# Kernel tuning notes

Measured on AMD Instinct MI355X. Metric: run time of the kernel, lower is better.

The kernel has to match this reference:

```python
import jax, jax.numpy as jnp
import numpy as np

B, L, W, C = 16, 200, 64, 128
H_INTRA = 64   # intra_hidden // 2 per direction
H_INTER = 128
EPS = 1e-8


def layer_norm(x, gamma, beta):
    mu = jnp.mean(x, axis=-1, keepdims=True)
    var = jnp.mean(jnp.square(x - mu), axis=-1, keepdims=True)
    return (x - mu) * jax.lax.rsqrt(var + EPS) * gamma + beta


def gru_seq(x, Wk, Uk, b, H):
    """Keras GRU, reset_after=False, recurrent_activation=sigmoid. x: [N,T,D] -> [N,T,H]."""
    xw = jnp.einsum('ntd,dk->ntk', x, Wk) + b  # precompute input projections [N,T,3H]
    def step(h, xw_t):
        z = jax.nn.sigmoid(xw_t[:, :H] + h @ Uk[:, :H])
        r = jax.nn.sigmoid(xw_t[:, H:2 * H] + h @ Uk[:, H:2 * H])
        hh = jnp.tanh(xw_t[:, 2 * H:] + (r * h) @ Uk[:, 2 * H:])
        h = z * h + (1.0 - z) * hh
        return h, h
    h0 = jnp.zeros((x.shape[0], H), x.dtype)
    _, ys = jax.lax.scan(step, h0, jnp.swapaxes(xw, 0, 1))  # [T,N,H]
    return jnp.swapaxes(ys, 0, 1)


def skip_gru_seq(x, Wk, Uk, b, Wp, bp, H):
    """Skip-RNN GRU (Campos et al.): binary update gate u_t conditionally updates state.
    Returns (outputs [N,T,H], gates [N,T,1])."""
    xw = jnp.einsum('ntd,dk->ntk', x, Wk) + b
    def step(carry, xw_t):
        h, ut = carry
        # straight-through binarization of cumulative update prob
        u = ut + jax.lax.stop_gradient(jnp.round(ut) - ut)  # [N,1]
        z = jax.nn.sigmoid(xw_t[:, :H] + h @ Uk[:, :H])
        r = jax.nn.sigmoid(xw_t[:, H:2 * H] + h @ Uk[:, H:2 * H])
        hh = jnp.tanh(xw_t[:, 2 * H:] + (r * h) @ Uk[:, 2 * H:])
        h_new = z * h + (1.0 - z) * hh
        h = u * h_new + (1.0 - u) * h  # skip: copy state when u == 0
        delta = jax.nn.sigmoid(h @ Wp + bp)  # [N,1]
        ut_next = u * delta + (1.0 - u) * (ut + jnp.minimum(delta, 1.0 - ut))
        return (h, ut_next), (h, u)
    N = x.shape[0]
    h0 = jnp.zeros((N, H), x.dtype)
    ut0 = jnp.ones((N, 1), x.dtype)
    _, (ys, us) = jax.lax.scan(step, (h0, ut0), jnp.swapaxes(xw, 0, 1))
    return jnp.swapaxes(ys, 0, 1), jnp.swapaxes(us, 0, 1)


def setup_inputs():
    key = jax.random.key(0)
    ks = jax.random.split(key, 16)
    rn = lambda k, s: jax.random.normal(k, s, dtype=jnp.float32) * 0.05
    z = lambda s: jnp.zeros(s, jnp.float32)
    o = lambda s: jnp.ones(s, jnp.float32)
    return {
        'x': jax.random.normal(ks[0], (B, L, W, C), dtype=jnp.float32),
        'scale': jax.random.uniform(ks[1], (B, L, W, 1), dtype=jnp.float32),
        'Wf': rn(ks[2], (C, 3 * H_INTRA)), 'Uf': rn(ks[3], (H_INTRA, 3 * H_INTRA)), 'bf': z((3 * H_INTRA,)),
        'Wb': rn(ks[4], (C, 3 * H_INTRA)), 'Ub': rn(ks[5], (H_INTRA, 3 * H_INTRA)), 'bb': z((3 * H_INTRA,)),
        'W_intra_fc': rn(ks[6], (2 * H_INTRA, C)), 'b_intra_fc': z((C,)),
        'g_intra': o((C,)), 'beta_intra': z((C,)),
        'Wi': rn(ks[7], (C + 1, 3 * H_INTER)), 'Ui': rn(ks[8], (H_INTER, 3 * H_INTER)), 'bi': z((3 * H_INTER,)),
        'Wp': rn(ks[9], (H_INTER, 1)), 'bp': z((1,)),
        'W_inter_fc': rn(ks[10], (H_INTER, C)), 'b_inter_fc': z((C,)),
        'g_inter': o((C,)), 'beta_inter': z((C,)),
    }


def reference(x, scale, Wf, Uf, bf, Wb, Ub, bb, W_intra_fc, b_intra_fc, g_intra, beta_intra,
              Wi, Ui, bi, Wp, bp, W_inter_fc, b_inter_fc, g_inter, beta_inter):
    # ----- intra path: bidirectional GRU over the width axis -----
    intra_in = x.reshape(B * L, W, C)
    out_f = gru_seq(intra_in, Wf, Uf, bf, H_INTRA)
    out_b = gru_seq(intra_in[:, ::-1, :], Wb, Ub, bb, H_INTRA)[:, ::-1, :]
    intra_rnn_out = jnp.concatenate([out_f, out_b], axis=-1)  # [B*L, W, 2H]
    update_gate_intra = jnp.ones((64, L), jnp.float32)  # skip=0 branch: constant ones
    intra_dense = intra_rnn_out @ W_intra_fc + b_intra_fc  # [B*L, W, C]
    intra_out = x + layer_norm(intra_dense.reshape(B, L, W, C), g_intra, beta_intra)
    # ----- inter path: skip-GRU over the L (time) axis -----
    inter_in = jnp.transpose(intra_out, (0, 2, 1, 3)).reshape(B * W, L, C)
    scale2 = jnp.transpose(scale, (0, 2, 1, 3)).reshape(B * W, L, 1)
    inter_in = jnp.concatenate([inter_in, scale2], axis=-1)  # [B*W, L, C+1]
    inter_rnn_out, gates = skip_gru_seq(inter_in, Wi, Ui, bi, Wp, bp, H_INTER)
    update_gate_inter = gates[:, :, 0]  # [B*W, L]
    inter_dense = (inter_rnn_out @ W_inter_fc + b_inter_fc).reshape(B, W, L, C)
    inter_ln_in = jnp.transpose(inter_dense, (0, 2, 1, 3))  # [B, L, W, C]
    inter_out = intra_out + layer_norm(inter_ln_in, g_inter, beta_inter)
    return inter_out, update_gate_intra, update_gate_inter
```

## Files before the change

### kernel.cpp

```cpp
#include <hip/hip_runtime.h>
#include <cmath>


__device__ __forceinline__ float sigf(float x) { return 1.0f / (1.0f + expf(-x)); }

__global__ __launch_bounds__(256) void k_fill_ones(float* __restrict__ p, int n) {
  int i = blockIdx.x * 256 + threadIdx.x;
  if (i < n) p[i] = 1.0f;
}

enum { MA_X_FWD = 0, MA_X_BWD = 1, MA_INTER = 2 };

template <int MODE>
__global__ __launch_bounds__(256) void k_gemm_xw(
    const float* __restrict__ A0, const float* __restrict__ A1,
    const float* __restrict__ Bm, const float* __restrict__ bias,
    float* __restrict__ Cm, long M0, int N, int K, int KT)
{
  __shared__ float As[16][68];
  __shared__ float Bs[16][68];
  const int tid = threadIdx.x;
  const int tx = tid & 15, ty = tid >> 4;
  const long row0g = M0 + (long)blockIdx.x * 64;
  const int col0 = blockIdx.y * 64;
  const int lr = tid >> 2;
  const int lk4 = (tid & 3) * 4;
  const int bk = tid >> 4;
  const int bc4 = (tid & 15) * 4;
  float acc[4][4];
#pragma unroll
  for (int i = 0; i < 4; ++i)
#pragma unroll
    for (int j = 0; j < 4; ++j) acc[i][j] = 0.f;

  for (int kt = 0; kt < KT; ++kt) {
    const int k0 = kt * 16;
    {
      const long rg = row0g + lr;
      float v0, v1, v2, v3;
      if (MODE == MA_X_FWD) {
        const float4 a4 = *reinterpret_cast<const float4*>(&A0[rg * 128 + k0 + lk4]);
        v0 = a4.x; v1 = a4.y; v2 = a4.z; v3 = a4.w;
      } else if (MODE == MA_X_BWD) {
        const long s = rg >> 6; const int t = (int)(rg & 63);
        const float4 a4 =
            *reinterpret_cast<const float4*>(&A0[(s * 64 + (63 - t)) * 128 + k0 + lk4]);
        v0 = a4.x; v1 = a4.y; v2 = a4.z; v3 = a4.w;
      } else {
        const int n = (int)(rg & 1023);
        const int l = (int)(rg >> 10);
        const long rowc = ((long)(n >> 6) * 200 + l) * 64 + (n & 63);
        const long base = rowc * 128;
        float vv[4];
#pragma unroll
        for (int i = 0; i < 4; ++i) {
          const int k = k0 + lk4 + i;
          vv[i] = (k < 128) ? A0[base + k] : ((k == 128) ? A1[rowc] : 0.f);
        }
        v0 = vv[0]; v1 = vv[1]; v2 = vv[2]; v3 = vv[3];
      }
      As[lk4 + 0][lr] = v0;
      As[lk4 + 1][lr] = v1;
      As[lk4 + 2][lr] = v2;
      As[lk4 + 3][lr] = v3;
    }
    {
      const int k = k0 + bk;
      float4 b4 = make_float4(0.f, 0.f, 0.f, 0.f);
      if (k < K) b4 = *reinterpret_cast<const float4*>(&Bm[(long)k * N + col0 + bc4]);
      *reinterpret_cast<float4*>(&Bs[bk][bc4]) = b4;
    }
    __syncthreads();
#pragma unroll
    for (int kk = 0; kk < 16; ++kk) {
      const float4 a4 = *reinterpret_cast<const float4*>(&As[kk][ty * 4]);
      const float4 b4 = *reinterpret_cast<const float4*>(&Bs[kk][tx * 4]);
      const float av[4] = {a4.x, a4.y, a4.z, a4.w};
      const float bv[4] = {b4.x, b4.y, b4.z, b4.w};
#pragma unroll
      for (int i = 0; i < 4; ++i)
#pragma unroll
        for (int j = 0; j < 4; ++j) acc[i][j] = fmaf(av[i], bv[j], acc[i][j]);
    }
    __syncthreads();
  }
  const float4 bi4 = *reinterpret_cast<const float4*>(&bias[col0 + tx * 4]);
  const float bv[4] = {bi4.x, bi4.y, bi4.z, bi4.w};
#pragma unroll
  for (int i = 0; i < 4; ++i) {
    const long rl = (long)blockIdx.x * 64 + ty * 4 + i;
    float4 o;
    o.x = acc[i][0] + bv[0];
    o.y = acc[i][1] + bv[1];
    o.z = acc[i][2] + bv[2];
    o.w = acc[i][3] + bv[3];
    *reinterpret_cast<float4*>(&Cm[rl * (long)N + col0 + tx * 4]) = o;
  }
}

__global__ __launch_bounds__(256, 2) void k_gru_intra(
    const float* __restrict__ xwf, const float* __restrict__ xwb,
    const float* __restrict__ Uf, const float* __restrict__ Ub,
    float* __restrict__ rnn, int nseq)
{
  const int dir = blockIdx.y;
  const float* __restrict__ xw = dir ? xwb : xwf;
  const float* __restrict__ U = dir ? Ub : Uf;
  __shared__ float Us[64 * 192];
  __shared__ float hs[8][64];
  __shared__ float zs[8][64];
  __shared__ float rhs[8][64];
  const int tid = threadIdx.x;
#pragma unroll
  for (int i = 0; i < 12; ++i) {
    *reinterpret_cast<float4*>(&Us[(tid + i * 256) * 4]) =
        *reinterpret_cast<const float4*>(&U[(tid + i * 256) * 4]);
  }
  reinterpret_cast<float*>(hs)[tid] = 0.f;
  reinterpret_cast<float*>(hs)[tid + 256] = 0.f;
  __syncthreads();
  const int sA = tid >> 5;
  const int cA = tid & 31;
  const long s0 = (long)blockIdx.x * 8;
  const long xbase = (s0 + sA) * 64;
  float4 xzr = *reinterpret_cast<const float4*>(&xw[(xbase + 0) * 192 + 4 * cA]);
  float2 xh = *reinterpret_cast<const float2*>(&xw[(xbase + 0) * 192 + 128 + 2 * cA]);
  for (int t = 0; t < 64; ++t) {
    float4 xzr_n = make_float4(0.f, 0.f, 0.f, 0.f);
    float2 xh_n = make_float2(0.f, 0.f);
    if (t < 63) {
      xzr_n = *reinterpret_cast<const float4*>(&xw[(xbase + t + 1) * 192 + 4 * cA]);
      xh_n = *reinterpret_cast<const float2*>(&xw[(xbase + t + 1) * 192 + 128 + 2 * cA]);
    }
    float a0 = 0.f, a1 = 0.f, a2 = 0.f, a3 = 0.f;
#pragma unroll
    for (int k4 = 0; k4 < 16; ++k4) {
      const float4 h4 = *reinterpret_cast<const float4*>(&hs[sA][4 * k4]);
      const float hv[4] = {h4.x, h4.y, h4.z, h4.w};
#pragma unroll
      for (int i = 0; i < 4; ++i) {
        const float4 u4 =
            *reinterpret_cast<const float4*>(&Us[(4 * k4 + i) * 192 + 4 * cA]);
        a0 = fmaf(hv[i], u4.x, a0);
        a1 = fmaf(hv[i], u4.y, a1);
        a2 = fmaf(hv[i], u4.z, a2);
        a3 = fmaf(hv[i], u4.w, a3);
      }
    }
    if (cA < 16) {
      float4 zq;
      zq.x = sigf(xzr.x + a0);
      zq.y = sigf(xzr.y + a1);
      zq.z = sigf(xzr.z + a2);
      zq.w = sigf(xzr.w + a3);
      *reinterpret_cast<float4*>(&zs[sA][4 * cA]) = zq;
    } else {
      const int j0 = 4 * cA - 64;
      const float4 h4 = *reinterpret_cast<const float4*>(&hs[sA][j0]);
      float4 rq;
      rq.x = sigf(xzr.x + a0) * h4.x;
      rq.y = sigf(xzr.y + a1) * h4.y;
      rq.z = sigf(xzr.z + a2) * h4.z;
      rq.w = sigf(xzr.w + a3) * h4.w;
      *reinterpret_cast<float4*>(&rhs[sA][j0]) = rq;
    }
    __syncthreads();
    float b0 = 0.f, b1 = 0.f;
#pragma unroll
    for (int k4 = 0; k4 < 16; ++k4) {
      const float4 r4 = *reinterpret_cast<const float4*>(&rhs[sA][4 * k4]);
      const float rv[4] = {r4.x, r4.y, r4.z, r4.w};
#pragma unroll
      for (int i = 0; i < 4; ++i) {
        const float2 u2 =
            *reinterpret_cast<const float2*>(&Us[(4 * k4 + i) * 192 + 128 + 2 * cA]);
        b0 = fmaf(rv[i], u2.x, b0);
        b1 = fmaf(rv[i], u2.y, b1);
      }
    }
    {
      const int j0 = 2 * cA;
      const float hh0 = tanhf(xh.x + b0);
      const float hh1 = tanhf(xh.y + b1);
      const float z0 = zs[sA][j0], z1 = zs[sA][j0 + 1];
      const float ho0 = hs[sA][j0], ho1 = hs[sA][j0 + 1];
      const float hn0 = z0 * ho0 + (1.f - z0) * hh0;
      const float hn1 = z1 * ho1 + (1.f - z1) * hh1;
      hs[sA][j0] = hn0;
      hs[sA][j0 + 1] = hn1;
      const int tt = dir ? (63 - t) : t;
      float2 st; st.x = hn0; st.y = hn1;
      *reinterpret_cast<float2*>(
          &rnn[((s0 + sA) * 64 + tt) * 128 + dir * 64 + j0]) = st;
    }
    __syncthreads();
    xzr = xzr_n; xh = xh_n;
  }
}

__global__ __launch_bounds__(512, 4) void k_gru_inter2(
    const float* __restrict__ xw, const float* __restrict__ Ui,
    const float* __restrict__ Wp, const float* __restrict__ bp,
    float* __restrict__ rnn, float* __restrict__ gates,
    float* __restrict__ hstate, float* __restrict__ ustate,
    int t0, int nt)
{
  __shared__ float Uh[128 * 128];
  __shared__ float h_s[2][128];
  __shared__ float z_s[2][128];
  __shared__ float rh_s[2][128];
  __shared__ float wp_s[128];
  __shared__ float pred[2][4];
  __shared__ float ut_s[2];
  __shared__ float u_s[2];
  const int tid = threadIdx.x;
  const int w = tid >> 6, lane = tid & 63, half = lane >> 5, lcol = lane & 31;
  const int n0 = blockIdx.x * 2;
  const int colA = w * 32 + lcol;
  const int ksA = half;
  const int seqB = w >> 2;
  const int colB = (w & 3) * 32 + lcol;
  const int ksB = half;

  float uzr[64];
#pragma unroll
  for (int k = 0; k < 64; ++k) uzr[k] = Ui[(long)(ksA * 64 + k) * 384 + colA];

  for (int idx = tid; idx < 16384; idx += 512) {
    const int k = idx >> 7, c = idx & 127;
    const float v = Ui[(long)k * 384 + 256 + c];
    Uh[c * 128 + (((k >> 2) ^ (c & 31)) << 2) + (k & 3)] = v;
  }
  if (tid < 256) {
    const int s = tid >> 7, c = tid & 127;
    h_s[s][c] = (t0 == 0) ? 0.f : hstate[(long)(n0 + s) * 128 + c];
  }
  if (tid < 128) wp_s[tid] = Wp[tid];
  if (tid < 2) {
    ut_s[tid] = (t0 == 0) ? 1.0f : ustate[n0 + tid];
    u_s[tid] = (t0 == 0) ? 1.0f : ustate[1024 + n0 + tid];
  }
  const float bp0 = bp[0];
  __syncthreads();

  float xa0 = 0.f, xa1 = 0.f, xb0 = 0.f;
  if (lane < 32) {
    xa0 = xw[(long)n0 * 384 + colA];
    xa1 = xw[(long)(n0 + 1) * 384 + colA];
    xb0 = xw[(long)(n0 + seqB) * 384 + 256 + colB];
  }

  for (int dl = 0; dl < nt; ++dl) {
    const int dn = (dl + 1 < nt) ? dl + 1 : dl;
    float xa0n = 0.f, xa1n = 0.f, xbn = 0.f;
    if (lane < 32) {
      xa0n = xw[((long)dn * 1024 + n0) * 384 + colA];
      xa1n = xw[((long)dn * 1024 + n0 + 1) * 384 + colA];
      xbn = xw[((long)dn * 1024 + n0 + seqB) * 384 + 256 + colB];
    }
    float a0 = 0.f, a1 = 0.f;
    const int hb = ksA * 64;
#pragma unroll
    for (int k4 = 0; k4 < 16; ++k4) {
      const float4 h0 = *reinterpret_cast<const float4*>(&h_s[0][hb + 4 * k4]);
      const float4 h1 = *reinterpret_cast<const float4*>(&h_s[1][hb + 4 * k4]);
      a0 = fmaf(h0.x, uzr[4 * k4 + 0], a0);
      a0 = fmaf(h0.y, uzr[4 * k4 + 1], a0);
      a0 = fmaf(h0.z, uzr[4 * k4 + 2], a0);
      a0 = fmaf(h0.w, uzr[4 * k4 + 3], a0);
      a1 = fmaf(h1.x, uzr[4 * k4 + 0], a1);
      a1 = fmaf(h1.y, uzr[4 * k4 + 1], a1);
      a1 = fmaf(h1.z, uzr[4 * k4 + 2], a1);
      a1 = fmaf(h1.w, uzr[4 * k4 + 3], a1);
    }
    a0 += __shfl_xor(a0, 32);
    a1 += __shfl_xor(a1, 32);
    if (lane < 32) {
      const float p0 = xa0 + a0;
      const float p1 = xa1 + a1;
      if (colA < 128) {
        z_s[0][colA] = sigf(p0);
        z_s[1][colA] = sigf(p1);
      } else {
        const int c = colA - 128;
        rh_s[0][c] = sigf(p0) * h_s[0][c];
        rh_s[1][c] = sigf(p1) * h_s[1][c];
      }
    }
    __syncthreads();
    float b = 0.f;
    const int rb = ksB * 64;
#pragma unroll
    for (int k4 = 0; k4 < 16; ++k4) {
      const float4 r4 = *reinterpret_cast<const float4*>(&rh_s[seqB][rb + 4 * k4]);
      const int chunk = ((ksB << 4) + k4) ^ (colB & 31);
      const float4 u4 = *reinterpret_cast<const float4*>(&Uh[colB * 128 + (chunk << 2)]);
      b = fmaf(r4.x, u4.x, b);
      b = fmaf(r4.y, u4.y, b);
      b = fmaf(r4.z, u4.z, b);
      b = fmaf(r4.w, u4.w, b);
    }
    b += __shfl_xor(b, 32);
    if (lane < 32) {
      const float pre = xb0 + b;
      const float hh = tanhf(pre);
      const float z = z_s[seqB][colB];
      const float ho = h_s[seqB][colB];
      const float hn = z * ho + (1.f - z) * hh;
      const float u = u_s[seqB];
      const float hq = u * hn + (1.f - u) * ho;
      rnn[((long)dl * 1024 + n0 + seqB) * 128 + colB] = hq;
      h_s[seqB][colB] = hq;
      float p = hq * wp_s[colB];
      p += __shfl_xor(p, 16);
      p += __shfl_xor(p, 8);
      p += __shfl_xor(p, 4);
      p += __shfl_xor(p, 2);
      p += __shfl_xor(p, 1);
      if (lcol == 0) pred[seqB][w & 3] = p;
    }
    __syncthreads();
    if (tid < 2) {
      const float pp = pred[tid][0] + pred[tid][1] + pred[tid][2] + pred[tid][3];
      const float delta = sigf(pp + bp0);
      const float u = u_s[tid], ut = ut_s[tid];
      gates[(long)(n0 + tid) * 200 + t0 + dl] = u;
      const float utn = u * delta + (1.f - u) * (ut + fminf(delta, 1.f - ut));
      ut_s[tid] = utn;
      u_s[tid] = rintf(utn);
    }
    xa0 = xa0n; xa1 = xa1n; xb0 = xbn;
  }
  if (tid < 256) {
    const int s = tid >> 7, c = tid & 127;
    hstate[(long)(n0 + s) * 128 + c] = h_s[s][c];
  }
  if (tid < 2) {
    ustate[n0 + tid] = ut_s[tid];
    ustate[1024 + n0 + tid] = u_s[tid];
  }
}

template <int OM>
__global__ __launch_bounds__(256) void k_fcln(
    const float* __restrict__ A, const float* __restrict__ Wt,
    const float* __restrict__ bias, const float* __restrict__ gamma,
    const float* __restrict__ beta, const float* __restrict__ resid,
    float* __restrict__ dst, long M0)
{
  __shared__ float As[16][36];
  __shared__ float Bs[16][132];
  __shared__ float red0[32][33];
  __shared__ float red1[32][33];
  __shared__ float mu_s[32];
  __shared__ float rs_s[32];
  const int tid = threadIdx.x;
  const int tx = tid & 31, ty = tid >> 5;
  const long r0l = (long)blockIdx.x * 32;
  const int lr = tid >> 3;
  const int lk2 = (tid & 7) * 2;
  const int bkk = tid >> 4;
  const int bc8 = (tid & 15) * 8;
  float acc[4][4];
#pragma unroll
  for (int i = 0; i < 4; ++i)
#pragma unroll
    for (int j = 0; j < 4; ++j) acc[i][j] = 0.f;

  for (int kt = 0; kt < 8; ++kt) {
    const int k0 = kt * 16;
    const float2 a2 = *reinterpret_cast<const float2*>(&A[(r0l + lr) * 128 + k0 + lk2]);
    As[lk2][lr] = a2.x;
    As[lk2 + 1][lr] = a2.y;
    const float4 w0 = *reinterpret_cast<const float4*>(&Wt[(long)(k0 + bkk) * 128 + bc8]);
    const float4 w1 = *reinterpret_cast<const float4*>(&Wt[(long)(k0 + bkk) * 128 + bc8 + 4]);
    *reinterpret_cast<float4*>(&Bs[bkk][bc8]) = w0;
    *reinterpret_cast<float4*>(&Bs[bkk][bc8 + 4]) = w1;
    __syncthreads();
#pragma unroll
    for (int kk = 0; kk < 16; ++kk) {
      const float4 a4 = *reinterpret_cast<const float4*>(&As[kk][ty * 4]);
      const float4 b4 = *reinterpret_cast<const float4*>(&Bs[kk][tx * 4]);
      const float av[4] = {a4.x, a4.y, a4.z, a4.w};
      const float bv[4] = {b4.x, b4.y, b4.z, b4.w};
#pragma unroll
      for (int i = 0; i < 4; ++i)
#pragma unroll
        for (int j = 0; j < 4; ++j) acc[i][j] = fmaf(av[i], bv[j], acc[i][j]);
    }
    __syncthreads();
  }
  {
    const float4 bb4 = *reinterpret_cast<const float4*>(&bias[tx * 4]);
    const float bv[4] = {bb4.x, bb4.y, bb4.z, bb4.w};
#pragma unroll
    for (int i = 0; i < 4; ++i)
#pragma unroll
      for (int j = 0; j < 4; ++j) acc[i][j] += bv[j];
  }
#pragma unroll
  for (int i = 0; i < 4; ++i) {
    const float s = acc[i][0] + acc[i][1] + acc[i][2] + acc[i][3];
    const float q = acc[i][0] * acc[i][0] + acc[i][1] * acc[i][1] +
                    acc[i][2] * acc[i][2] + acc[i][3] * acc[i][3];
    red0[ty * 4 + i][tx] = s;
    red1[ty * 4 + i][tx] = q;
  }
  __syncthreads();
  if (tid < 32) {
    float s = 0.f, q = 0.f;
#pragma unroll
    for (int j = 0; j < 32; ++j) { s += red0[tid][j]; q += red1[tid][j]; }
    const float mu = s * (1.0f / 128.0f);
    const float var = q * (1.0f / 128.0f) - mu * mu;
    mu_s[tid] = mu;
    rs_s[tid] = 1.0f / sqrtf(var + 1e-8f);
  }
  __syncthreads();
  const float4 g4 = *reinterpret_cast<const float4*>(&gamma[tx * 4]);
  const float4 be4 = *reinterpret_cast<const float4*>(&beta[tx * 4]);
#pragma unroll
  for (int i = 0; i < 4; ++i) {
    const int rloc = ty * 4 + i;
    const long rg = M0 + r0l + rloc;
    long off;
    if (OM == 0) {
      off = rg * 128 + tx * 4;
    } else {
      const int n = (int)(rg & 1023);
      const int l = (int)(rg >> 10);
      off = (((long)(n >> 6) * 200 + l) * 64 + (n & 63)) * 128 + tx * 4;
    }
    const float4 r4 = *reinterpret_cast<const float4*>(&resid[off]);
    const float mu = mu_s[rloc], rs = rs_s[rloc];
    float4 o;
    o.x = (acc[i][0] - mu) * rs * g4.x + be4.x + r4.x;
    o.y = (acc[i][1] - mu) * rs * g4.y + be4.y + r4.y;
    o.z = (acc[i][2] - mu) * rs * g4.z + be4.z + r4.z;
    o.w = (acc[i][3] - mu) * rs * g4.w + be4.w + r4.w;
    *reinterpret_cast<float4*>(&dst[off]) = o;
  }
}

extern "C" void kernel_launch(void* const* d_in, const int* in_sizes, int n_in,
                              void* d_out, int out_size, void* d_ws, size_t ws_size,
                              hipStream_t stream)
{
  (void)in_sizes; (void)n_in; (void)out_size;
  const float* x    = (const float*)d_in[0];
  const float* scl  = (const float*)d_in[1];
  const float* Wf   = (const float*)d_in[2];
  const float* Uf   = (const float*)d_in[3];
  const float* bf   = (const float*)d_in[4];
  const float* Wb   = (const float*)d_in[5];
  const float* Ub   = (const float*)d_in[6];
  const float* bb   = (const float*)d_in[7];
  const float* Wfc1 = (const float*)d_in[8];
  const float* bfc1 = (const float*)d_in[9];
  const float* gam1 = (const float*)d_in[10];
  const float* bet1 = (const float*)d_in[11];
  const float* Wi   = (const float*)d_in[12];
  const float* Ui   = (const float*)d_in[13];
  const float* bi   = (const float*)d_in[14];
  const float* Wp   = (const float*)d_in[15];
  const float* bp   = (const float*)d_in[16];
  const float* Wfc2 = (const float*)d_in[17];
  const float* bfc2 = (const float*)d_in[18];
  const float* gam2 = (const float*)d_in[19];
  const float* bet2 = (const float*)d_in[20];

  float* outp  = (float*)d_out;
  float* io    = outp;
  float* onesp = outp + 26214400L;
  float* gates = outp + 26214400L + 12800L;
  float* ws    = (float*)d_ws;
  const long wsf = (long)(ws_size / sizeof(float));

  k_fill_ones<<<50, 256, 0, stream>>>(onesp, 12800);

  long cnI = (wsf / 32768L) & ~7L;
  if (cnI > 3200) cnI = 3200;
  if (cnI < 8) cnI = 8;
  for (long s0 = 0; s0 < 3200; s0 += cnI) {
    const long cn = (3200 - s0 < cnI) ? (3200 - s0) : cnI;
    float* xwf = ws;
    float* xwb = ws + cn * 12288L;
    float* rnn = ws + cn * 24576L;
    const long M = cn * 64;
    dim3 gg((unsigned)(M / 64), 3);
    k_gemm_xw<MA_X_FWD><<<gg, 256, 0, stream>>>(x, nullptr, Wf, bf, xwf, s0 * 64, 192, 128, 8);
    k_gemm_xw<MA_X_BWD><<<gg, 256, 0, stream>>>(x, nullptr, Wb, bb, xwb, s0 * 64, 192, 128, 8);
    dim3 gr((unsigned)(cn / 8), 2);
    k_gru_intra<<<gr, 256, 0, stream>>>(xwf, xwb, Uf, Ub, rnn, (int)cn);
    k_fcln<0><<<(unsigned)(M / 32), 256, 0, stream>>>(rnn, Wfc1, bfc1, gam1, bet1, x, io, s0 * 64);
  }

  const long per_t = 1024L * 384 + 1024L * 128;
  const long state_f = 1024L * 128 + 2048L;
  long nt_alloc = (wsf - state_f) / per_t;
  if (nt_alloc > 200) nt_alloc = 200;
  if (nt_alloc < 1) nt_alloc = 1;
  float* xwi    = ws;
  float* rnnI   = ws + nt_alloc * 1024L * 384;
  float* hstate = rnnI + nt_alloc * 1024L * 128;
  float* ustate = hstate + 1024L * 128;

  for (long t0 = 0; t0 < 200; t0 += nt_alloc) {
    const int nt = (int)((200 - t0 < nt_alloc) ? (200 - t0) : nt_alloc);
    dim3 gg((unsigned)(16 * nt), 6);
    k_gemm_xw<MA_INTER><<<gg, 256, 0, stream>>>(io, scl, Wi, bi, xwi, t0 * 1024, 384, 129, 9);
    k_gru_inter2<<<512, 512, 0, stream>>>(xwi, Ui, Wp, bp, rnnI, gates, hstate, ustate,
                                          (int)t0, nt);
    k_fcln<1><<<(unsigned)(32 * nt), 256, 0, stream>>>(rnnI, Wfc2, bfc2, gam2, bet2, io, outp,
                                                       t0 * 1024);
  }
}
```

Baseline: 2.112 ms.

## Rewrite GRU recurrences with register-resident weights and readlane broadcast of state

Both recurrent kernels now keep the recurrent weight slices in per-wave registers and broadcast hidden-state elements across lanes with readlane, instead of streaming the weights from shared memory. K is split across waves and the partial sums are reduced through shared memory. The intra kernel handles 4 sequences per block. The inter kernel handles 4 sequences per block with 1024 threads and skips the matmuls for sequences whose binary update gate is zero. The inter input GEMM also replaces per-element guarded loads with vector loads, and the state workspace size is adjusted. In exchange there are more barriers per step and heavy register pressure (64 weight floats per thread), which may limit occupancy.

```diff
diff --git a/kernel.cpp b/kernel.cpp
--- a/kernel.cpp
+++ b/kernel.cpp
@@ -3,6 +3,9 @@
 
 
 __device__ __forceinline__ float sigf(float x) { return 1.0f / (1.0f + expf(-x)); }
+__device__ __forceinline__ float rlanef(float v, int l) {
+  return __uint_as_float(__builtin_amdgcn_readlane(__float_as_uint(v), (unsigned)l));
+}
 
 __global__ __launch_bounds__(256) void k_fill_ones(float* __restrict__ p, int n) {
   int i = blockIdx.x * 256 + threadIdx.x;
@@ -51,13 +54,13 @@
         const int l = (int)(rg >> 10);
         const long rowc = ((long)(n >> 6) * 200 + l) * 64 + (n & 63);
         const long base = rowc * 128;
-        float vv[4];
-#pragma unroll
-        for (int i = 0; i < 4; ++i) {
-          const int k = k0 + lk4 + i;
-          vv[i] = (k < 128) ? A0[base + k] : ((k == 128) ? A1[rowc] : 0.f);
-        }
-        v0 = vv[0]; v1 = vv[1]; v2 = vv[2]; v3 = vv[3];
+        if (kt < 8) {
+          const float4 a4 = *reinterpret_cast<const float4*>(&A0[base + k0 + lk4]);
+          v0 = a4.x; v1 = a4.y; v2 = a4.z; v3 = a4.w;
+        } else {
+          v0 = (lk4 == 0) ? A1[rowc] : 0.f;
+          v1 = 0.f; v2 = 0.f; v3 = 0.f;
+        }
       }
       As[lk4 + 0][lr] = v0;
       As[lk4 + 1][lr] = v1;
@@ -98,246 +101,284 @@
   }
 }
 
-__global__ __launch_bounds__(256, 2) void k_gru_intra(
+__global__ __launch_bounds__(256, 4) void k_gru_intra2(
     const float* __restrict__ xwf, const float* __restrict__ xwb,
     const float* __restrict__ Uf, const float* __restrict__ Ub,
-    float* __restrict__ rnn, int nseq)
+    float* __restrict__ rnn)
 {
   const int dir = blockIdx.y;
   const float* __restrict__ xw = dir ? xwb : xwf;
-  const float* __restrict__ U = dir ? Ub : Uf;
-  __shared__ float Us[64 * 192];
-  __shared__ float hs[8][64];
-  __shared__ float zs[8][64];
-  __shared__ float rhs[8][64];
+  const float* __restrict__ U  = dir ? Ub : Uf;
+  __shared__ float h8[4][64], z8[4][64], rh8[4][64];
+  __shared__ float pA[4][2][128];
+  __shared__ float pB[4][2][64];
   const int tid = threadIdx.x;
-#pragma unroll
-  for (int i = 0; i < 12; ++i) {
-    *reinterpret_cast<float4*>(&Us[(tid + i * 256) * 4]) =
-        *reinterpret_cast<const float4*>(&U[(tid + i * 256) * 4]);
-  }
-  reinterpret_cast<float*>(hs)[tid] = 0.f;
-  reinterpret_cast<float*>(hs)[tid + 256] = 0.f;
+  const int w = tid >> 6, lane = tid & 63;
+  const long s0 = (long)blockIdx.x * 4;
+  const bool isZR = (w < 2);
+  const int ksZ = w;
+  const int ksH = w - 2;
+
+  float ua[32], ub[32];
+  if (isZR) {
+#pragma unroll
+    for (int k = 0; k < 32; ++k) {
+      ua[k] = U[(ksZ * 32 + k) * 192 + lane];
+      ub[k] = U[(ksZ * 32 + k) * 192 + 64 + lane];
+    }
+  } else {
+#pragma unroll
+    for (int k = 0; k < 32; ++k)
+      ua[k] = U[(ksH * 32 + k) * 192 + 128 + lane];
+  }
+  h8[w][lane] = 0.f;
   __syncthreads();
-  const int sA = tid >> 5;
-  const int cA = tid & 31;
-  const long s0 = (long)blockIdx.x * 8;
-  const long xbase = (s0 + sA) * 64;
-  float4 xzr = *reinterpret_cast<const float4*>(&xw[(xbase + 0) * 192 + 4 * cA]);
-  float2 xh = *reinterpret_cast<const float2*>(&xw[(xbase + 0) * 192 + 128 + 2 * cA]);
+
+  const long xrow0 = (s0 + w) * 64;
+  float xa1 = xw[xrow0 * 192 + lane];
+  float xa2 = xw[xrow0 * 192 + 64 + lane];
+  float xb  = xw[xrow0 * 192 + 128 + lane];
+
   for (int t = 0; t < 64; ++t) {
-    float4 xzr_n = make_float4(0.f, 0.f, 0.f, 0.f);
-    float2 xh_n = make_float2(0.f, 0.f);
-    if (t < 63) {
-      xzr_n = *reinterpret_cast<const float4*>(&xw[(xbase + t + 1) * 192 + 4 * cA]);
-      xh_n = *reinterpret_cast<const float2*>(&xw[(xbase + t + 1) * 192 + 128 + 2 * cA]);
-    }
-    float a0 = 0.f, a1 = 0.f, a2 = 0.f, a3 = 0.f;
-#pragma unroll
-    for (int k4 = 0; k4 < 16; ++k4) {
-      const float4 h4 = *reinterpret_cast<const float4*>(&hs[sA][4 * k4]);
-      const float hv[4] = {h4.x, h4.y, h4.z, h4.w};
-#pragma unroll
-      for (int i = 0; i < 4; ++i) {
-        const float4 u4 =
-            *reinterpret_cast<const float4*>(&Us[(4 * k4 + i) * 192 + 4 * cA]);
-        a0 = fmaf(hv[i], u4.x, a0);
-        a1 = fmaf(hv[i], u4.y, a1);
-        a2 = fmaf(hv[i], u4.z, a2);
-        a3 = fmaf(hv[i], u4.w, a3);
-      }
-    }
-    if (cA < 16) {
-      float4 zq;
-      zq.x = sigf(xzr.x + a0);
-      zq.y = sigf(xzr.y + a1);
-      zq.z = sigf(xzr.z + a2);
-      zq.w = sigf(xzr.w + a3);
-      *reinterpret_cast<float4*>(&zs[sA][4 * cA]) = zq;
-    } else {
-      const int j0 = 4 * cA - 64;
-      const float4 h4 = *reinterpret_cast<const float4*>(&hs[sA][j0]);
-      float4 rq;
-      rq.x = sigf(xzr.x + a0) * h4.x;
-      rq.y = sigf(xzr.y + a1) * h4.y;
-      rq.z = sigf(xzr.z + a2) * h4.z;
-      rq.w = sigf(xzr.w + a3) * h4.w;
-      *reinterpret_cast<float4*>(&rhs[sA][j0]) = rq;
-    }
-    __syncthreads();
-    float b0 = 0.f, b1 = 0.f;
-#pragma unroll
-    for (int k4 = 0; k4 < 16; ++k4) {
-      const float4 r4 = *reinterpret_cast<const float4*>(&rhs[sA][4 * k4]);
-      const float rv[4] = {r4.x, r4.y, r4.z, r4.w};
-#pragma unroll
-      for (int i = 0; i < 4; ++i) {
-        const float2 u2 =
-            *reinterpret_cast<const float2*>(&Us[(4 * k4 + i) * 192 + 128 + 2 * cA]);
-        b0 = fmaf(rv[i], u2.x, b0);
-        b1 = fmaf(rv[i], u2.y, b1);
-      }
-    }
+    const int tn = (t < 63) ? t + 1 : t;
+    const float xa1n = xw[(xrow0 + tn) * 192 + lane];
+    const float xa2n = xw[(xrow0 + tn) * 192 + 64 + lane];
+    const float xbn  = xw[(xrow0 + tn) * 192 + 128 + lane];
+    if (isZR) {
+      const float hv0 = h8[lane >> 5][ksZ * 32 + (lane & 31)];
+      const float hv1 = h8[2 + (lane >> 5)][ksZ * 32 + (lane & 31)];
+      float az[4], ar[4];
+#pragma unroll
+      for (int s = 0; s < 4; ++s) { az[s] = 0.f; ar[s] = 0.f; }
+#pragma unroll
+      for (int s = 0; s < 4; ++s) {
+        const float hvr = (s < 2) ? hv0 : hv1;
+#pragma unroll
+        for (int k = 0; k < 32; ++k) {
+          const float hs = rlanef(hvr, ((s & 1) << 5) | k);
+          az[s] = fmaf(ua[k], hs, az[s]);
+          ar[s] = fmaf(ub[k], hs, ar[s]);
+        }
+      }
+#pragma unroll
+      for (int s = 0; s < 4; ++s) {
+        pA[s][ksZ][lane] = az[s];
+        pA[s][ksZ][64 + lane] = ar[s];
+      }
+    }
+    __syncthreads();
     {
-      const int j0 = 2 * cA;
-      const float hh0 = tanhf(xh.x + b0);
-      const float hh1 = tanhf(xh.y + b1);
-      const float z0 = zs[sA][j0], z1 = zs[sA][j0 + 1];
-      const float ho0 = hs[sA][j0], ho1 = hs[sA][j0 + 1];
-      const float hn0 = z0 * ho0 + (1.f - z0) * hh0;
-      const float hn1 = z1 * ho1 + (1.f - z1) * hh1;
-      hs[sA][j0] = hn0;
-      hs[sA][j0 + 1] = hn1;
+      const float sz = pA[w][0][lane] + pA[w][1][lane] + xa1;
+      const float sr = pA[w][0][64 + lane] + pA[w][1][64 + lane] + xa2;
+      z8[w][lane] = sigf(sz);
+      rh8[w][lane] = sigf(sr) * h8[w][lane];
+    }
+    __syncthreads();
+    if (!isZR) {
+      const float rv0 = rh8[lane >> 5][ksH * 32 + (lane & 31)];
+      const float rv1 = rh8[2 + (lane >> 5)][ksH * 32 + (lane & 31)];
+      float ah[4];
+#pragma unroll
+      for (int s = 0; s < 4; ++s) ah[s] = 0.f;
+#pragma unroll
+      for (int s = 0; s < 4; ++s) {
+        const float rvr = (s < 2) ? rv0 : rv1;
+#pragma unroll
+        for (int k = 0; k < 32; ++k) {
+          const float rs = rlanef(rvr, ((s & 1) << 5) | k);
+          ah[s] = fmaf(ua[k], rs, ah[s]);
+        }
+      }
+#pragma unroll
+      for (int s = 0; s < 4; ++s) pB[s][ksH][lane] = ah[s];
+    }
+    __syncthreads();
+    {
+      const float pre = pB[w][0][lane] + pB[w][1][lane] + xb;
+      const float hh = tanhf(pre);
+      const float z = z8[w][lane];
+      const float ho = h8[w][lane];
+      const float hn = z * ho + (1.f - z) * hh;
+      h8[w][lane] = hn;
       const int tt = dir ? (63 - t) : t;
-      float2 st; st.x = hn0; st.y = hn1;
-      *reinterpret_cast<float2*>(
-          &rnn[((s0 + sA) * 64 + tt) * 128 + dir * 64 + j0]) = st;
-    }
-    __syncthreads();
-    xzr = xzr_n; xh = xh_n;
-  }
-}
-
-__global__ __launch_bounds__(512, 4) void k_gru_inter2(
+      rnn[((s0 + w) * 64 + tt) * 128 + dir * 64 + lane] = hn;
+    }
+    __syncthreads();
+    xa1 = xa1n; xa2 = xa2n; xb = xbn;
+  }
+}
+
+__global__ __launch_bounds__(1024, 4) void k_gru_inter3(
     const float* __restrict__ xw, const float* __restrict__ Ui,
     const float* __restrict__ Wp, const float* __restrict__ bp,
     float* __restrict__ rnn, float* __restrict__ gates,
     float* __restrict__ hstate, float* __restrict__ ustate,
     int t0, int nt)
 {
-  __shared__ float Uh[128 * 128];
-  __shared__ float h_s[2][128];
-  __shared__ float z_s[2][128];
-  __shared__ float rh_s[2][128];
-  __shared__ float wp_s[128];
-  __shared__ float pred[2][4];
-  __shared__ float ut_s[2];
-  __shared__ float u_s[2];
+  __shared__ float h4[4][128], z4[4][128], rh4[4][128];
+  __shared__ float pA[4][8][256];
+  __shared__ float pB[4][8][128];
+  __shared__ float uu[4], utt[4];
   const int tid = threadIdx.x;
-  const int w = tid >> 6, lane = tid & 63, half = lane >> 5, lcol = lane & 31;
-  const int n0 = blockIdx.x * 2;
-  const int colA = w * 32 + lcol;
-  const int ksA = half;
-  const int seqB = w >> 2;
-  const int colB = (w & 3) * 32 + lcol;
-  const int ksB = half;
-
-  float uzr[64];
-#pragma unroll
-  for (int k = 0; k < 64; ++k) uzr[k] = Ui[(long)(ksA * 64 + k) * 384 + colA];
-
-  for (int idx = tid; idx < 16384; idx += 512) {
-    const int k = idx >> 7, c = idx & 127;
-    const float v = Ui[(long)k * 384 + 256 + c];
-    Uh[c * 128 + (((k >> 2) ^ (c & 31)) << 2) + (k & 3)] = v;
-  }
-  if (tid < 256) {
+  const int w = tid >> 6, lane = tid & 63;
+  const int n0 = blockIdx.x * 4;
+  const bool isZR = (w < 8);
+
+  float ureg[64];
+  if (isZR) {
+#pragma unroll
+    for (int j = 0; j < 4; ++j)
+#pragma unroll
+      for (int k = 0; k < 16; ++k)
+        ureg[j * 16 + k] = Ui[(long)(w * 16 + k) * 384 + j * 64 + lane];
+  } else {
+    const int ks = w - 8;
+#pragma unroll
+    for (int j = 0; j < 2; ++j)
+#pragma unroll
+      for (int k = 0; k < 16; ++k)
+        ureg[j * 16 + k] = Ui[(long)(ks * 16 + k) * 384 + 256 + j * 64 + lane];
+  }
+  if (tid < 512) {
     const int s = tid >> 7, c = tid & 127;
-    h_s[s][c] = (t0 == 0) ? 0.f : hstate[(long)(n0 + s) * 128 + c];
-  }
-  if (tid < 128) wp_s[tid] = Wp[tid];
-  if (tid < 2) {
-    ut_s[tid] = (t0 == 0) ? 1.0f : ustate[n0 + tid];
-    u_s[tid] = (t0 == 0) ? 1.0f : ustate[1024 + n0 + tid];
+    h4[s][c] = (t0 == 0) ? 0.f : hstate[(long)(n0 + s) * 128 + c];
+  }
+  if (tid < 4) {
+    utt[tid] = (t0 == 0) ? 1.f : ustate[n0 + tid];
+    uu[tid]  = (t0 == 0) ? 1.f : ustate[1024 + n0 + tid];
   }
   const float bp0 = bp[0];
+  float wprA = 0.f, wprB = 0.f;
+  if (w < 4) { wprA = Wp[lane]; wprB = Wp[64 + lane]; }
   __syncthreads();
 
-  float xa0 = 0.f, xa1 = 0.f, xb0 = 0.f;
-  if (lane < 32) {
-    xa0 = xw[(long)n0 * 384 + colA];
-    xa1 = xw[(long)(n0 + 1) * 384 + colA];
-    xb0 = xw[(long)(n0 + seqB) * 384 + 256 + colB];
+  const int cs = w >> 2;
+  const int cc = (w & 3) * 64 + lane;
+  float xc = xw[(long)(n0 + cs) * 384 + cc];
+  float xbA = 0.f, xbB = 0.f;
+  if (w < 4) {
+    xbA = xw[(long)(n0 + w) * 384 + 256 + lane];
+    xbB = xw[(long)(n0 + w) * 384 + 320 + lane];
   }
 
   for (int dl = 0; dl < nt; ++dl) {
+    const float u0g = uu[0], u1g = uu[1], u2g = uu[2], u3g = uu[3];
+    const bool act = (u0g + u1g + u2g + u3g) != 0.f;
     const int dn = (dl + 1 < nt) ? dl + 1 : dl;
-    float xa0n = 0.f, xa1n = 0.f, xbn = 0.f;
-    if (lane < 32) {
-      xa0n = xw[((long)dn * 1024 + n0) * 384 + colA];
-      xa1n = xw[((long)dn * 1024 + n0 + 1) * 384 + colA];
-      xbn = xw[((long)dn * 1024 + n0 + seqB) * 384 + 256 + colB];
-    }
-    float a0 = 0.f, a1 = 0.f;
-    const int hb = ksA * 64;
-#pragma unroll
-    for (int k4 = 0; k4 < 16; ++k4) {
-      const float4 h0 = *reinterpret_cast<const float4*>(&h_s[0][hb + 4 * k4]);
-      const float4 h1 = *reinterpret_cast<const float4*>(&h_s[1][hb + 4 * k4]);
-      a0 = fmaf(h0.x, uzr[4 * k4 + 0], a0);
-      a0 = fmaf(h0.y, uzr[4 * k4 + 1], a0);
-      a0 = fmaf(h0.z, uzr[4 * k4 + 2], a0);
-      a0 = fmaf(h0.w, uzr[4 * k4 + 3], a0);
-      a1 = fmaf(h1.x, uzr[4 * k4 + 0], a1);
-      a1 = fmaf(h1.y, uzr[4 * k4 + 1], a1);
-      a1 = fmaf(h1.z, uzr[4 * k4 + 2], a1);
-      a1 = fmaf(h1.w, uzr[4 * k4 + 3], a1);
-    }
-    a0 += __shfl_xor(a0, 32);
-    a1 += __shfl_xor(a1, 32);
-    if (lane < 32) {
-      const float p0 = xa0 + a0;
-      const float p1 = xa1 + a1;
-      if (colA < 128) {
-        z_s[0][colA] = sigf(p0);
-        z_s[1][colA] = sigf(p1);
+    const float xcn = xw[((long)dn * 1024 + n0 + cs) * 384 + cc];
+    float xbAn = 0.f, xbBn = 0.f;
+    if (w < 4) {
+      xbAn = xw[((long)dn * 1024 + n0 + w) * 384 + 256 + lane];
+      xbBn = xw[((long)dn * 1024 + n0 + w) * 384 + 320 + lane];
+    }
+    if (act) {
+      if (isZR) {
+        const float hv = h4[lane >> 4][w * 16 + (lane & 15)];
+        float acc[4][4];
+#pragma unroll
+        for (int j = 0; j < 4; ++j)
+#pragma unroll
+          for (int s = 0; s < 4; ++s) acc[j][s] = 0.f;
+#pragma unroll
+        for (int s = 0; s < 4; ++s) {
+          const float ug = (s == 0) ? u0g : (s == 1) ? u1g : (s == 2) ? u2g : u3g;
+          if (ug != 0.f) {
+#pragma unroll
+            for (int k = 0; k < 16; ++k) {
+              const float hs = rlanef(hv, (s << 4) | k);
+              acc[0][s] = fmaf(ureg[k], hs, acc[0][s]);
+              acc[1][s] = fmaf(ureg[16 + k], hs, acc[1][s]);
+              acc[2][s] = fmaf(ureg[32 + k], hs, acc[2][s]);
+              acc[3][s] = fmaf(ureg[48 + k], hs, acc[3][s]);
+            }
+#pragma unroll
+            for (int j = 0; j < 4; ++j) pA[s][w][j * 64 + lane] = acc[j][s];
+          }
+        }
+      }
+      __syncthreads();
+      {
+        const float ugc = uu[cs];
+        if (ugc != 0.f) {
+          float sum = xc;
+#pragma unroll
+          for (int ks = 0; ks < 8; ++ks) sum += pA[cs][ks][cc];
+          if (cc < 128) z4[cs][cc] = sigf(sum);
+          else rh4[cs][cc - 128] = sigf(sum) * h4[cs][cc - 128];
+        }
+      }
+      __syncthreads();
+      if (!isZR) {
+        const int ks = w - 8;
+        const float rv = rh4[lane >> 4][ks * 16 + (lane & 15)];
+        float acc0[4], acc1[4];
+#pragma unroll
+        for (int s = 0; s < 4; ++s) { acc0[s] = 0.f; acc1[s] = 0.f; }
+#pragma unroll
+        for (int s = 0; s < 4; ++s) {
+          const float ug = (s == 0) ? u0g : (s == 1) ? u1g : (s == 2) ? u2g : u3g;
+          if (ug != 0.f) {
+#pragma unroll
+            for (int k = 0; k < 16; ++k) {
+              const float rs = rlanef(rv, (s << 4) | k);
+              acc0[s] = fmaf(ureg[k], rs, acc0[s]);
+              acc1[s] = fmaf(ureg[16 + k], rs, acc1[s]);
+            }
+            pB[s][ks][lane] = acc0[s];
+            pB[s][ks][64 + lane] = acc1[s];
+          }
+        }
+      }
+      __syncthreads();
+    }
+    if (w < 4) {
+      const float us = uu[w];
+      const float hoA = h4[w][lane], hoB = h4[w][64 + lane];
+      float hqA, hqB;
+      if (us != 0.f) {
+        float sA = xbA, sB = xbB;
+#pragma unroll
+        for (int ks = 0; ks < 8; ++ks) {
+          sA += pB[w][ks][lane];
+          sB += pB[w][ks][64 + lane];
+        }
+        const float hhA = tanhf(sA), hhB = tanhf(sB);
+        const float zA = z4[w][lane], zB = z4[w][64 + lane];
+        hqA = zA * hoA + (1.f - zA) * hhA;
+        hqB = zB * hoB + (1.f - zB) * hhB;
+        h4[w][lane] = hqA;
+        h4[w][64 + lane] = hqB;
       } else {
-        const int c = colA - 128;
-        rh_s[0][c] = sigf(p0) * h_s[0][c];
-        rh_s[1][c] = sigf(p1) * h_s[1][c];
-      }
-    }
-    __syncthreads();
-    float b = 0.f;
-    const int rb = ksB * 64;
-#pragma unroll
-    for (int k4 = 0; k4 < 16; ++k4) {
-      const float4 r4 = *reinterpret_cast<const float4*>(&rh_s[seqB][rb + 4 * k4]);
-      const int chunk = ((ksB << 4) + k4) ^ (colB & 31);
-      const float4 u4 = *reinterpret_cast<const float4*>(&Uh[colB * 128 + (chunk << 2)]);
-      b = fmaf(r4.x, u4.x, b);
-      b = fmaf(r4.y, u4.y, b);
-      b = fmaf(r4.z, u4.z, b);
-      b = fmaf(r4.w, u4.w, b);
-    }
-    b += __shfl_xor(b, 32);
-    if (lane < 32) {
-      const float pre = xb0 + b;
-      const float hh = tanhf(pre);
-      const float z = z_s[seqB][colB];
-      const float ho = h_s[seqB][colB];
-      const float hn = z * ho + (1.f - z) * hh;
-      const float u = u_s[seqB];
-      const float hq = u * hn + (1.f - u) * ho;
-      rnn[((long)dl * 1024 + n0 + seqB) * 128 + colB] = hq;
-      h_s[seqB][colB] = hq;
-      float p = hq * wp_s[colB];
+        hqA = hoA; hqB = hoB;
+      }
+      rnn[((long)dl * 1024 + n0 + w) * 128 + lane] = hqA;
+      rnn[((long)dl * 1024 + n0 + w) * 128 + 64 + lane] = hqB;
+      float p = hqA * wprA + hqB * wprB;
+      p += __shfl_xor(p, 32);
       p += __shfl_xor(p, 16);
       p += __shfl_xor(p, 8);
       p += __shfl_xor(p, 4);
       p += __shfl_xor(p, 2);
       p += __shfl_xor(p, 1);
-      if (lcol == 0) pred[seqB][w & 3] = p;
-    }
-    __syncthreads();
-    if (tid < 2) {
-      const float pp = pred[tid][0] + pred[tid][1] + pred[tid][2] + pred[tid][3];
-      const float delta = sigf(pp + bp0);
-      const float u = u_s[tid], ut = ut_s[tid];
-      gates[(long)(n0 + tid) * 200 + t0 + dl] = u;
-      const float utn = u * delta + (1.f - u) * (ut + fminf(delta, 1.f - ut));
-      ut_s[tid] = utn;
-      u_s[tid] = rintf(utn);
-    }
-    xa0 = xa0n; xa1 = xa1n; xb0 = xbn;
-  }
-  if (tid < 256) {
+      const float delta = sigf(p + bp0);
+      const float ut = utt[w];
+      const float utn = us * delta + (1.f - us) * (ut + fminf(delta, 1.f - ut));
+      if (lane == 0) {
+        gates[(long)(n0 + w) * 200 + t0 + dl] = us;
+        utt[w] = utn;
+        uu[w] = rintf(utn);
+      }
+    }
+    __syncthreads();
+    xc = xcn; xbA = xbAn; xbB = xbBn;
+  }
+  if (tid < 512) {
     const int s = tid >> 7, c = tid & 127;
-    hstate[(long)(n0 + s) * 128 + c] = h_s[s][c];
-  }
-  if (tid < 2) {
-    ustate[n0 + tid] = ut_s[tid];
-    ustate[1024 + n0 + tid] = u_s[tid];
+    hstate[(long)(n0 + s) * 128 + c] = h4[s][c];
+  }
+  if (tid < 4) {
+    ustate[n0 + tid] = utt[tid];
+    ustate[1024 + n0 + tid] = uu[tid];
   }
 }
 
@@ -490,13 +531,13 @@
     dim3 gg((unsigned)(M / 64), 3);
     k_gemm_xw<MA_X_FWD><<<gg, 256, 0, stream>>>(x, nullptr, Wf, bf, xwf, s0 * 64, 192, 128, 8);
     k_gemm_xw<MA_X_BWD><<<gg, 256, 0, stream>>>(x, nullptr, Wb, bb, xwb, s0 * 64, 192, 128, 8);
-    dim3 gr((unsigned)(cn / 8), 2);
-    k_gru_intra<<<gr, 256, 0, stream>>>(xwf, xwb, Uf, Ub, rnn, (int)cn);
+    dim3 gr((unsigned)(cn / 4), 2);
+    k_gru_intra2<<<gr, 256, 0, stream>>>(xwf, xwb, Uf, Ub, rnn);
     k_fcln<0><<<(unsigned)(M / 32), 256, 0, stream>>>(rnn, Wfc1, bfc1, gam1, bet1, x, io, s0 * 64);
   }
 
   const long per_t = 1024L * 384 + 1024L * 128;
-  const long state_f = 1024L * 128 + 2048L;
+  const long state_f = 1024L * 128 + 3072L;
   long nt_alloc = (wsf - state_f) / per_t;
   if (nt_alloc > 200) nt_alloc = 200;
   if (nt_alloc < 1) nt_alloc = 1;
@@ -509,8 +550,8 @@
     const int nt = (int)((200 - t0 < nt_alloc) ? (200 - t0) : nt_alloc);
     dim3 gg((unsigned)(16 * nt), 6);
     k_gemm_xw<MA_INTER><<<gg, 256, 0, stream>>>(io, scl, Wi, bi, xwi, t0 * 1024, 384, 129, 9);
-    k_gru_inter2<<<512, 512, 0, stream>>>(xwi, Ui, Wp, bp, rnnI, gates, hstate, ustate,
-                                          (int)t0, nt);
+    k_gru_inter3<<<256, 1024, 0, stream>>>(xwi, Ui, Wp, bp, rnnI, gates, hstate, ustate,
+                                           (int)t0, nt);
     k_fcln<1><<<(unsigned)(32 * nt), 256, 0, stream>>>(rnnI, Wfc2, bfc2, gam2, bet2, io, outp,
                                                        t0 * 1024);
   }
```

Measured after the change: 1.884 ms. 10.8% less time.
